# Performance work log

Hardware: AMD Instinct MI355X
Metric: run time of the kernel (lower is better)

## Reference

```python
import jax, jax.numpy as jnp
import numpy as np

M1, M2, M3 = 12, 12, 8
WIDTH = 32


def _spectral_conv(v, wr, wi):
    # v: [B, C, X, Y, T]; wr/wi: [4, Ci, Co, M1, M2, M3]
    B, C, X, Y, T = v.shape
    vft = jnp.fft.rfftn(v, axes=(-3, -2, -1))  # [B,C,X,Y,T//2+1] complex
    w = wr.astype(jnp.complex64) + 1j * wi.astype(jnp.complex64)
    mul = lambda blk, ww: jnp.einsum('bixyz,ioxyz->boxyz', blk, ww)
    out = jnp.zeros((B, wr.shape[2], X, Y, T // 2 + 1), dtype=vft.dtype)
    out = out.at[:, :, :M1, :M2, :M3].set(mul(vft[:, :, :M1, :M2, :M3], w[0]))
    out = out.at[:, :, -M1:, :M2, :M3].set(mul(vft[:, :, -M1:, :M2, :M3], w[1]))
    out = out.at[:, :, :M1, -M2:, :M3].set(mul(vft[:, :, :M1, -M2:, :M3], w[2]))
    out = out.at[:, :, -M1:, -M2:, :M3].set(mul(vft[:, :, -M1:, -M2:, :M3], w[3]))
    return jnp.fft.irfftn(out, s=(X, Y, T), axes=(-3, -2, -1))


def _conv1x1(v, w, b):
    # v: [B,C,X,Y,T]; w: [Co,Ci]; b: [Co]
    return jnp.einsum('bixyz,oi->boxyz', v, w) + b[None, :, None, None, None]


def setup_inputs() -> dict:
    key = jax.random.key(0)
    ks = jax.random.split(key, 24)
    B, X, Y, T = 8, 64, 64, 40
    W = WIDTH
    scale = 1.0 / (W * W)
    d = {}
    d['h'] = jax.random.normal(ks[0], (B, X, Y, T, 2), dtype=jnp.float32)
    d['x'] = jax.random.normal(ks[1], (B, X, Y, T, 3), dtype=jnp.float32)
    d['fc0_w'] = jax.random.normal(ks[2], (5, W), dtype=jnp.float32) * 0.3
    d['fc0_b'] = jnp.zeros((W,), dtype=jnp.float32)
    for i, name in enumerate(['sc0', 'sc1', 'sc3']):
        d[name + '_wr'] = scale * jax.random.uniform(ks[3 + 2 * i], (4, W, W, M1, M2, M3), dtype=jnp.float32)
        d[name + '_wi'] = scale * jax.random.uniform(ks[4 + 2 * i], (4, W, W, M1, M2, M3), dtype=jnp.float32)
    for i, name in enumerate(['w0', 'w1', 'w3']):
        d[name + '_w'] = jax.random.normal(ks[9 + 2 * i], (W, W), dtype=jnp.float32) * (1.0 / np.sqrt(W))
        d[name + '_b'] = jnp.zeros((W,), dtype=jnp.float32)
    d['fc1_w'] = jax.random.normal(ks[15], (W, 64), dtype=jnp.float32) * (1.0 / np.sqrt(W))
    d['fc1_b'] = jnp.zeros((64,), dtype=jnp.float32)
    d['fc2_w'] = jax.random.normal(ks[16], (64, 2), dtype=jnp.float32) * 0.125
    d['fc2_b'] = jnp.zeros((2,), dtype=jnp.float32)
    return d


def reference(h, x, fc0_w, fc0_b, sc0_wr, sc0_wi, sc1_wr, sc1_wi, sc3_wr, sc3_wi,
              w0_w, w0_b, w1_w, w1_b, w3_w, w3_b, fc1_w, fc1_b, fc2_w, fc2_b):
    v = jnp.concatenate((h, x), axis=-1)                 # [B,X,Y,T,5]
    v = v @ fc0_w + fc0_b                                # lift to width
    v = jnp.transpose(v, (0, 4, 1, 2, 3))                # [B,W,X,Y,T]
    v = jax.nn.gelu(_spectral_conv(v, sc0_wr, sc0_wi) + _conv1x1(v, w0_w, w0_b), approximate=False)
    v = jax.nn.gelu(_spectral_conv(v, sc1_wr, sc1_wi) + _conv1x1(v, w1_w, w1_b), approximate=False)
    v = _spectral_conv(v, sc3_wr, sc3_wi) + _conv1x1(v, w3_w, w3_b)
    v = jnp.transpose(v, (0, 2, 3, 4, 1))                # [B,X,Y,T,W]
    v = jax.nn.gelu(v @ fc1_w + fc1_b, approximate=False)
    return v @ fc2_w + fc2_b                             # [B,X,Y,T,2]
```

## Files before the change

### kernel.cpp

```cpp
#include <hip/hip_runtime.h>
#include <math.h>

#define BATCH 8
#define WID   32
#define NX    64
#define NY    64
#define NT    40
#define M1C   12
#define KT    8
#define KXC   24
#define KYC   24
#define NXY   (NX*NY)
#define NXYT  (NXY*NT)
#define NP    (BATCH*NXYT)

#define TWO_PI 6.283185307179586f

static __device__ __forceinline__ float gelu_f(float v){
  return 0.5f*v*(1.0f + erff(v*0.7071067811865476f));
}

static __device__ __forceinline__ void barrier_lds(){
  asm volatile("s_waitcnt lgkmcnt(0)\n\ts_barrier" ::: "memory");
}


__global__ __launch_bounds__(256) void k_fc0(const float* __restrict__ h, const float* __restrict__ x,
                                             const float* __restrict__ w, const float* __restrict__ b,
                                             float* __restrict__ V){
  __shared__ float sw[160], sb[32];
  int tid=threadIdx.x;
  if(tid<160) sw[tid]=w[tid];
  if(tid<32)  sb[tid]=b[tid];
  __syncthreads();
  int pl = tid>>3, q = tid&7;
  int p = blockIdx.x*32 + pl;
  float i0=h[(size_t)p*2], i1=h[(size_t)p*2+1];
  float i2=x[(size_t)p*3], i3=x[(size_t)p*3+1], i4=x[(size_t)p*3+2];
  int c0=q*4;
  float4 o;
  float* po=(float*)&o;
  #pragma unroll
  for(int u=0;u<4;u++){
    int c=c0+u;
    po[u] = sb[c] + i0*sw[c] + i1*sw[32+c] + i2*sw[64+c] + i3*sw[96+c] + i4*sw[128+c];
  }
  ((float4*)V)[(size_t)p*8 + q] = o;
}

__global__ __launch_bounds__(256) void k_fwd_ty(const float* __restrict__ V, float2* __restrict__ F2){
  __shared__ __align__(16) unsigned char smem[61696];
  float*  vt    = (float*)smem;
  float2* f2out = (float2*)smem;
  float2* twy   = (float2*)(smem + 49408);
  int tid = threadIdx.x;
  int b = blockIdx.x >> 6, x = blockIdx.x & 63;
  int c = tid & 31, k = tid >> 5;
  for(int i=tid;i<KYC*NY;i+=256){
    int ky=i/NY, y=i-ky*NY;
    int f = ky<M1C ? ky : ky+40;
    float ang = -TWO_PI*(float)((f*y)%NY)/(float)NY;
    twy[ky*NY+y] = make_float2(cosf(ang), sinf(ang));
  }
  float2 twr[NT];
  #pragma unroll
  for(int t=0;t<NT;t++){
    float ang = -TWO_PI*(float)((k*t)%NT)/(float)NT;
    twr[t] = make_float2(cosf(ang), sinf(ang));
  }
  float2 acc[KYC];
  #pragma unroll
  for(int ky=0;ky<KYC;ky++) acc[ky]=make_float2(0.f,0.f);
  const float4* src = (const float4*)(V + (size_t)(b*NX+x)*(NY*NT*WID));
  for(int g=0; g<8; g++){
    __syncthreads();
    #pragma unroll
    for(int r=0;r<10;r++) ((float4*)vt)[r*256+tid] = src[g*2560 + r*256 + tid];
    __syncthreads();
    for(int yl=0; yl<8; yl+=2){
      float sr0=0.f, si0=0.f, sr1=0.f, si1=0.f;
      const float* vp0 = vt + yl*1280 + c;
      const float* vp1 = vp0 + 1280;
      #pragma unroll
      for(int t=0;t<NT;t++){
        float2 w = twr[t];
        float v0 = vp0[t*32];
        float v1 = vp1[t*32];
        sr0 += v0*w.x; si0 += v0*w.y;
        sr1 += v1*w.x; si1 += v1*w.y;
      }
      int y = g*8 + yl;
      #pragma unroll
      for(int ky=0;ky<KYC;ky++){
        float4 wy = *(const float4*)&twy[ky*NY + y];
        acc[ky].x += sr0*wy.x - si0*wy.y + sr1*wy.z - si1*wy.w;
        acc[ky].y += sr0*wy.y + si0*wy.x + sr1*wy.w + si1*wy.z;
      }
    }
  }
  __syncthreads();
  #pragma unroll
  for(int ky=0;ky<KYC;ky++) f2out[c*193 + ky*KT + k] = acc[ky];
  __syncthreads();
  for(int i=tid;i<WID*KYC*KT;i+=256){
    int cc=i/192, e=i-cc*192;
    F2[((size_t)(b*WID+cc)*NX + x)*(KYC*KT) + e] = f2out[cc*193 + e];
  }
}

__global__ __launch_bounds__(256) void k_fwd_x(const float2* __restrict__ F2, float2* __restrict__ F3){
  __shared__ float2 tile[NX*KT];
  __shared__ float2 twi[KXC*65];
  int tid=threadIdx.x;
  int bc = blockIdx.x / KYC;
  int ky = blockIdx.x - bc*KYC;
  for(int i=tid;i<NX*KT;i+=256){
    int xx=i/KT, kt=i-xx*KT;
    tile[i] = F2[((size_t)bc*NX + xx)*(KYC*KT) + ky*KT + kt];
  }
  for(int i=tid;i<KXC*NX;i+=256){
    int kx=i/NX, xx=i-kx*NX;
    int f = kx<M1C ? kx : kx+40;
    float ang = -TWO_PI*(float)((f*xx)%NX)/(float)NX;
    twi[kx*65+xx] = make_float2(cosf(ang), sinf(ang));
  }
  __syncthreads();
  for(int item=tid; item<KXC*KT; item+=256){
    int kx=item/KT, kt=item-kx*KT;
    float sr=0.f, si=0.f;
    #pragma unroll 8
    for(int xx=0;xx<NX;xx++){
      float2 a = tile[xx*KT+kt];
      float2 w = twi[kx*65+xx];
      sr += a.x*w.x - a.y*w.y;
      si += a.x*w.y + a.y*w.x;
    }
    F3[(size_t)bc*(KXC*KYC*KT) + kx*(KYC*KT) + ky*KT + kt] = make_float2(sr,si);
  }
}

__global__ __launch_bounds__(256) void k_mix(const float2* __restrict__ F3, const float* __restrict__ wr,
                                             const float* __restrict__ wi, float2* __restrict__ F4){
  __shared__ float2 f3s[BATCH*WID*KT];
  int tid = threadIdx.x;
  int kx = blockIdx.x / KYC, ky = blockIdx.x - kx*KYC;
  int mode0 = blockIdx.x * KT;
  int xp = (kx>=M1C), yp = (ky>=M1C);
  int m1 = kx - M1C*xp, m2 = ky - M1C*yp;
  int blk = xp + 2*yp;
  for(int i=tid;i<1024;i+=256){
    int row=i>>2, q=i&3;
    ((float4*)f3s)[row*4+q] = ((const float4*)(F3 + (size_t)row*4608 + mode0))[q];
  }
  int o = tid>>3, kt = tid&7;
  size_t wbase = (size_t)blk*1179648 + (size_t)o*1152 + m1*96 + m2*8 + kt;
  float wre[WID], wim[WID];
  #pragma unroll
  for(int i=0;i<WID;i++){
    wre[i] = wr[wbase + (size_t)i*36864];
    wim[i] = wi[wbase + (size_t)i*36864];
  }
  __syncthreads();
  #pragma unroll
  for(int b=0;b<BATCH;b++){
    float ar=0.f, ai=0.f;
    #pragma unroll
    for(int i=0;i<WID;i++){
      float2 a = f3s[(b*WID+i)*KT + kt];
      ar += a.x*wre[i] - a.y*wim[i];
      ai += a.x*wim[i] + a.y*wre[i];
    }
    F4[(size_t)(b*WID+o)*4608 + mode0 + kt] = make_float2(ar,ai);
  }
}

__global__ __launch_bounds__(256) void k_inv_x(const float2* __restrict__ F4, float2* __restrict__ F2){
  __shared__ float2 tile[KXC*KT];
  __shared__ float2 twi[NX*25];
  int tid=threadIdx.x;
  int bc = blockIdx.x / KYC, ky = blockIdx.x - (blockIdx.x/KYC)*KYC;
  for(int i=tid;i<KXC*KT;i+=256){
    int kx=i/KT, kt=i-kx*KT;
    tile[i] = F4[(size_t)bc*4608 + kx*(KYC*KT) + ky*KT + kt];
  }
  for(int i=tid;i<NX*KXC;i+=256){
    int xx=i/KXC, kx=i-xx*KXC;
    int f = kx<M1C ? kx : kx+40;
    float ang = TWO_PI*(float)((f*xx)%NX)/(float)NX;
    twi[xx*25+kx] = make_float2(cosf(ang)*(1.0f/64.0f), sinf(ang)*(1.0f/64.0f));
  }
  __syncthreads();
  for(int item=tid; item<NX*KT; item+=256){
    int xx=item/KT, kt=item-xx*KT;
    float sr=0.f, si=0.f;
    #pragma unroll 8
    for(int kx=0;kx<KXC;kx++){
      float2 a = tile[kx*KT+kt];
      float2 w = twi[xx*25+kx];
      sr += a.x*w.x - a.y*w.y;
      si += a.x*w.y + a.y*w.x;
    }
    F2[((size_t)bc*NX + xx)*(KYC*KT) + ky*KT + kt] = make_float2(sr,si);
  }
}

template<bool GELU>
__global__ __launch_bounds__(256) void k_conv(const float2* __restrict__ F2, const float* __restrict__ wcv,
                                              const float* __restrict__ bcv, float* __restrict__ V){
  __shared__ __align__(16) unsigned char smem[34816];
  float*  vtA  = (float*)smem;
  float*  vtB  = (float*)(smem+10240);
  float2* ftc0 = (float2*)(smem+20480);
  float2* ftc1 = (float2*)(smem+24576);
  float2* twy  = (float2*)(smem+28672);
  float2* f2h  = (float2*)smem;

  int tid=threadIdx.x;
  int b  = blockIdx.x >> 7;
  int x  = (blockIdx.x >> 1) & 63;
  int y0 = (blockIdx.x & 1) * 32;
  int cid = tid & 31, ktid = tid >> 5;
  int oid = tid & 31, tg  = tid >> 5;

  float2 fr[KYC];
  #pragma unroll
  for(int half=0; half<2; half++){
    for(int i=tid;i<1536;i+=256){
      int cc=i/96, q=i-cc*96;
      ((float4*)f2h)[i] = *((const float4*)(F2 + ((size_t)(b*WID + half*16 + cc)*NX + x)*(KYC*KT)) + q);
    }
    __syncthreads();
    if((cid>>4) == half){
      const float2* fp = f2h + (cid&15)*192 + ktid;
      #pragma unroll
      for(int ky=0;ky<KYC;ky++) fr[ky] = fp[ky*8];
    }
    __syncthreads();
  }
  {
    float ts = (ktid==0 ? 1.0f : 2.0f) * (1.0f/(float)NT);
    #pragma unroll
    for(int ky=0;ky<KYC;ky++){ fr[ky].x *= ts; fr[ky].y *= ts; }
  }
  float wreg[WID];
  #pragma unroll
  for(int cc=0;cc<WID;cc++) wreg[cc] = wcv[oid*WID + cc];
  float breg = bcv[oid];
  float2 twtg[KT];
  #pragma unroll
  for(int k=0;k<KT;k++){
    float ang = 0.78539816339744831f*(float)((k*tg)&7);
    twtg[k] = make_float2(cosf(ang), sinf(ang));
  }
  for(int i=tid;i<32*KYC;i+=256){
    int yy=i/KYC, ky=i-yy*KYC;
    int f = ky<M1C ? ky : ky+40;
    float ang = TWO_PI*(float)((f*(y0+yy))%NY)/(float)NY;
    twy[i] = make_float2(cosf(ang)*(1.0f/64.0f), sinf(ang)*(1.0f/64.0f));
  }
  float* plane = V + (size_t)((b*NX+x)*NY + y0)*(NT*WID);
  const float4* gp = (const float4*)plane;
  bool has3 = tid < 128;
  {
    float4 p0 = gp[tid], p1 = gp[256+tid];
    float4 p2 = has3 ? gp[512+tid] : make_float4(0,0,0,0);
    ((float4*)vtA)[tid] = p0;
    ((float4*)vtA)[256+tid] = p1;
    if(has3) ((float4*)vtA)[512+tid] = p2;
  }
  float4 rA = gp[640+tid], rB = gp[640+256+tid];
  float4 rC = has3 ? gp[640+512+tid] : make_float4(0,0,0,0);
  __syncthreads();

  constexpr float CJ[KT][5] = {
    {1.f, 1.f,          1.f,          1.f,          1.f         },
    {1.f, 0.98768834f,  0.95105652f,  0.89100652f,  0.80901699f },
    {1.f, 0.95105652f,  0.80901699f,  0.58778525f,  0.30901699f },
    {1.f, 0.89100652f,  0.58778525f,  0.15643447f, -0.30901699f },
    {1.f, 0.80901699f,  0.30901699f, -0.30901699f, -0.80901699f },
    {1.f, 0.70710678f,  0.f,         -0.70710678f, -1.f         },
    {1.f, 0.58778525f, -0.30901699f, -0.95105652f, -0.80901699f },
    {1.f, 0.45399050f, -0.58778525f, -0.98768834f, -0.30901699f },
  };
  constexpr float SJ[KT][5] = {
    {0.f, 0.f,          0.f,          0.f,          0.f         },
    {0.f, 0.15643447f,  0.30901699f,  0.45399050f,  0.58778525f },
    {0.f, 0.30901699f,  0.58778525f,  0.80901699f,  0.95105652f },
    {0.f, 0.45399050f,  0.80901699f,  0.98768834f,  0.95105652f },
    {0.f, 0.58778525f,  0.95105652f,  0.95105652f,  0.58778525f },
    {0.f, 0.70710678f,  1.f,          0.70710678f,  0.f         },
    {0.f, 0.80901699f,  0.95105652f,  0.30901699f, -0.58778525f },
    {0.f, 0.89100652f,  0.80901699f, -0.15643447f, -0.95105652f },
  };

  #pragma unroll 1
  for(int it=0; it<16; ++it){
    float*  vcur = (it&1) ? vtB  : vtA;
    float*  vnxt = (it&1) ? vtA  : vtB;
    float2* fcur = (it&1) ? ftc1 : ftc0;
    int yl = it*2;
    {
      const float2* tw0 = twy + (size_t)yl*KYC;
      const float2* tw1 = tw0 + KYC;
      float sr0=0.f, si0=0.f, sr1=0.f, si1=0.f;
      #pragma unroll
      for(int ky=0;ky<KYC;ky+=2){
        float2 a  = fr[ky];
        float2 b2 = fr[ky+1];
        float4 w0 = *(const float4*)&tw0[ky];
        float4 w1 = *(const float4*)&tw1[ky];
        sr0 += a.x*w0.x - a.y*w0.y + b2.x*w0.z - b2.y*w0.w;
        si0 += a.x*w0.y + a.y*w0.x + b2.x*w0.w + b2.y*w0.z;
        sr1 += a.x*w1.x - a.y*w1.y + b2.x*w1.z - b2.y*w1.w;
        si1 += a.x*w1.y + a.y*w1.x + b2.x*w1.w + b2.y*w1.z;
      }
      fcur[      ktid*32 + cid] = make_float2(sr0,si0);
      fcur[256 + ktid*32 + cid] = make_float2(sr1,si1);
    }
    barrier_lds();
    if(it+1 < 16){
      ((float4*)vnxt)[tid] = rA;
      ((float4*)vnxt)[256+tid] = rB;
      if(has3) ((float4*)vnxt)[512+tid] = rC;
    }
    if(it+2 < 16){
      const float4* q = gp + (size_t)(it+2)*640;
      rA = q[tid]; rB = q[256+tid];
      if(has3) rC = q[512+tid];
    }
    #pragma unroll
    for(int yy=0; yy<2; yy++){
      const float2* fsrc = fcur + yy*256;
      const float*  vb   = vcur + yy*1280;
      float* outp = plane + (size_t)(yl+yy)*(NT*WID);
      float acc[5];
      #pragma unroll
      for(int j=0;j<5;j++) acc[j] = breg;
      #pragma unroll
      for(int k=0;k<KT;k++){
        float2 f = fsrc[k*32 + oid];
        float gx = f.x*twtg[k].x - f.y*twtg[k].y;
        float gy = f.x*twtg[k].y + f.y*twtg[k].x;
        #pragma unroll
        for(int j=0;j<5;j++) acc[j] += gx*CJ[k][j] - gy*SJ[k][j];
      }
      #pragma unroll
      for(int j=0;j<5;j++){
        int t = tg*5 + j;
        float a = acc[j];
        const float* vrow = vb + t*32;
        #pragma unroll
        for(int c4=0;c4<WID;c4+=4){
          float4 vv = *(const float4*)(vrow + c4);
          a += vv.x*wreg[c4] + vv.y*wreg[c4+1] + vv.z*wreg[c4+2] + vv.w*wreg[c4+3];
        }
        outp[t*32 + oid] = GELU ? gelu_f(a) : a;
      }
    }
  }
}

__global__ __launch_bounds__(256) void k_mlp(const float* __restrict__ V, const float* __restrict__ w1,
                                             const float* __restrict__ b1, const float* __restrict__ w2,
                                             const float* __restrict__ b2, float* __restrict__ out){
  __shared__ float sw1t[64*WID];
  __shared__ float sb1[64], sw2[128], sb2[2];
  int tid=threadIdx.x;
  for(int i=tid;i<64*WID;i+=256){ int j=i>>5, c=i&31; sw1t[i]=w1[c*64+j]; }
  if(tid<64) sb1[tid]=b1[tid];
  if(tid<128) sw2[tid]=w2[tid];
  if(tid<2) sb2[tid]=b2[tid];
  __syncthreads();
  size_t p0 = (size_t)blockIdx.x*1024 + (size_t)tid*4;
  float vv[128];
  const float4* vp = (const float4*)(V + p0*WID);
  #pragma unroll
  for(int q=0;q<32;q++) *((float4*)(vv+4*q)) = vp[q];
  float oa[8];
  #pragma unroll
  for(int pt=0;pt<4;pt++){ oa[2*pt]=sb2[0]; oa[2*pt+1]=sb2[1]; }
  #pragma unroll 4
  for(int j=0;j<64;j++){
    float a0=sb1[j], a1=a0, a2=a0, a3=a0;
    const float* wrow = sw1t + j*WID;
    #pragma unroll
    for(int c4=0;c4<WID;c4+=4){
      float4 w = *(const float4*)(wrow + c4);
      a0 += vv[     c4]*w.x + vv[     c4+1]*w.y + vv[     c4+2]*w.z + vv[     c4+3]*w.w;
      a1 += vv[32 + c4]*w.x + vv[32 + c4+1]*w.y + vv[32 + c4+2]*w.z + vv[32 + c4+3]*w.w;
      a2 += vv[64 + c4]*w.x + vv[64 + c4+1]*w.y + vv[64 + c4+2]*w.z + vv[64 + c4+3]*w.w;
      a3 += vv[96 + c4]*w.x + vv[96 + c4+1]*w.y + vv[96 + c4+2]*w.z + vv[96 + c4+3]*w.w;
    }
    a0=gelu_f(a0); a1=gelu_f(a1); a2=gelu_f(a2); a3=gelu_f(a3);
    float u0=sw2[2*j], u1=sw2[2*j+1];
    oa[0]+=a0*u0; oa[1]+=a0*u1; oa[2]+=a1*u0; oa[3]+=a1*u1;
    oa[4]+=a2*u0; oa[5]+=a2*u1; oa[6]+=a3*u0; oa[7]+=a3*u1;
  }
  float4* op = (float4*)(out + p0*2);
  op[0]=make_float4(oa[0],oa[1],oa[2],oa[3]);
  op[1]=make_float4(oa[4],oa[5],oa[6],oa[7]);
}

extern "C" void kernel_launch(void* const* d_in, const int* in_sizes, int n_in,
                              void* d_out, int out_size, void* d_ws, size_t ws_size,
                              hipStream_t stream){
  const float* h     = (const float*)d_in[0];
  const float* x     = (const float*)d_in[1];
  const float* fc0_w = (const float*)d_in[2];
  const float* fc0_b = (const float*)d_in[3];
  const float* scwr[3] = {(const float*)d_in[4], (const float*)d_in[6], (const float*)d_in[8]};
  const float* scwi[3] = {(const float*)d_in[5], (const float*)d_in[7], (const float*)d_in[9]};
  const float* cw[3]   = {(const float*)d_in[10], (const float*)d_in[12], (const float*)d_in[14]};
  const float* cb[3]   = {(const float*)d_in[11], (const float*)d_in[13], (const float*)d_in[15]};
  const float* fc1_w = (const float*)d_in[16];
  const float* fc1_b = (const float*)d_in[17];
  const float* fc2_w = (const float*)d_in[18];
  const float* fc2_b = (const float*)d_in[19];

  const size_t VSZ = (size_t)BATCH*WID*NXYT;
  float*  V  = (float*)d_ws;
  float2* F2 = (float2*)(V + VSZ);
  float2* F4 = F2 + (size_t)BATCH*WID*NX*KYC*KT;
  float2* F3 = (float2*)d_out;

  k_fc0<<<NP/32, 256, 0, stream>>>(h, x, fc0_w, fc0_b, V);
  for(int L=0; L<3; L++){
    k_fwd_ty<<<BATCH*NX, 256, 0, stream>>>(V, F2);
    k_fwd_x<<<(BATCH*WID)*KYC, 256, 0, stream>>>(F2, F3);
    k_mix<<<KXC*KYC, 256, 0, stream>>>(F3, scwr[L], scwi[L], F4);
    k_inv_x<<<(BATCH*WID)*KYC, 256, 0, stream>>>(F4, F2);
    if(L<2) k_conv<true ><<<BATCH*NX*2, 256, 0, stream>>>(F2, cw[L], cb[L], V);
    else    k_conv<false><<<BATCH*NX*2, 256, 0, stream>>>(F2, cw[L], cb[L], V);
  }
  k_mlp<<<NP/1024, 256, 0, stream>>>(V, fc1_w, fc1_b, fc2_w, fc2_b, (float*)d_out);
}
```

Before: 1.555 ms.

## Split forward T/Y DFT across ky halves and fold T symmetry

```diff
diff --git a/kernel.cpp b/kernel.cpp
--- a/kernel.cpp
+++ b/kernel.cpp
@@ -49,62 +49,65 @@
 }
 
 __global__ __launch_bounds__(256) void k_fwd_ty(const float* __restrict__ V, float2* __restrict__ F2){
-  __shared__ __align__(16) unsigned char smem[61696];
+  __shared__ __align__(16) unsigned char smem[26624];
   float*  vt    = (float*)smem;
+  float2* twy   = (float2*)(smem + 20480);
   float2* f2out = (float2*)smem;
-  float2* twy   = (float2*)(smem + 49408);
   int tid = threadIdx.x;
-  int b = blockIdx.x >> 6, x = blockIdx.x & 63;
+  int b = blockIdx.x >> 7, x = (blockIdx.x >> 1) & 63, kyh = blockIdx.x & 1;
   int c = tid & 31, k = tid >> 5;
-  for(int i=tid;i<KYC*NY;i+=256){
-    int ky=i/NY, y=i-ky*NY;
+  for(int i=tid;i<12*NY;i+=256){
+    int kyl=i>>6, y=i&63;
+    int ky = kyh*12 + kyl;
     int f = ky<M1C ? ky : ky+40;
     float ang = -TWO_PI*(float)((f*y)%NY)/(float)NY;
-    twy[ky*NY+y] = make_float2(cosf(ang), sinf(ang));
-  }
-  float2 twr[NT];
-  #pragma unroll
-  for(int t=0;t<NT;t++){
+    twy[i] = make_float2(cosf(ang), sinf(ang));
+  }
+  float2 twr[20];
+  #pragma unroll
+  for(int t=0;t<20;t++){
     float ang = -TWO_PI*(float)((k*t)%NT)/(float)NT;
     twr[t] = make_float2(cosf(ang), sinf(ang));
   }
-  float2 acc[KYC];
-  #pragma unroll
-  for(int ky=0;ky<KYC;ky++) acc[ky]=make_float2(0.f,0.f);
+  float sgn = (k&1) ? -1.0f : 1.0f;
+  float2 acc[12];
+  #pragma unroll
+  for(int q=0;q<12;q++) acc[q]=make_float2(0.f,0.f);
   const float4* src = (const float4*)(V + (size_t)(b*NX+x)*(NY*NT*WID));
-  for(int g=0; g<8; g++){
+  for(int g=0; g<16; g++){
     __syncthreads();
     #pragma unroll
-    for(int r=0;r<10;r++) ((float4*)vt)[r*256+tid] = src[g*2560 + r*256 + tid];
+    for(int r=0;r<5;r++) ((float4*)vt)[r*256+tid] = src[g*1280 + r*256 + tid];
     __syncthreads();
-    for(int yl=0; yl<8; yl+=2){
+    #pragma unroll
+    for(int yl=0; yl<4; yl+=2){
       float sr0=0.f, si0=0.f, sr1=0.f, si1=0.f;
       const float* vp0 = vt + yl*1280 + c;
       const float* vp1 = vp0 + 1280;
       #pragma unroll
-      for(int t=0;t<NT;t++){
+      for(int t=0;t<20;t++){
         float2 w = twr[t];
-        float v0 = vp0[t*32];
-        float v1 = vp1[t*32];
-        sr0 += v0*w.x; si0 += v0*w.y;
-        sr1 += v1*w.x; si1 += v1*w.y;
+        float u0 = fmaf(sgn, vp0[(t+20)*32], vp0[t*32]);
+        float u1 = fmaf(sgn, vp1[(t+20)*32], vp1[t*32]);
+        sr0 += u0*w.x; si0 += u0*w.y;
+        sr1 += u1*w.x; si1 += u1*w.y;
       }
-      int y = g*8 + yl;
-      #pragma unroll
-      for(int ky=0;ky<KYC;ky++){
-        float4 wy = *(const float4*)&twy[ky*NY + y];
-        acc[ky].x += sr0*wy.x - si0*wy.y + sr1*wy.z - si1*wy.w;
-        acc[ky].y += sr0*wy.y + si0*wy.x + sr1*wy.w + si1*wy.z;
+      int y = g*4 + yl;
+      #pragma unroll
+      for(int q=0;q<12;q++){
+        float4 wy = *(const float4*)&twy[q*NY + y];
+        acc[q].x += sr0*wy.x - si0*wy.y + sr1*wy.z - si1*wy.w;
+        acc[q].y += sr0*wy.y + si0*wy.x + sr1*wy.w + si1*wy.z;
       }
     }
   }
   __syncthreads();
   #pragma unroll
-  for(int ky=0;ky<KYC;ky++) f2out[c*193 + ky*KT + k] = acc[ky];
-  __syncthreads();
-  for(int i=tid;i<WID*KYC*KT;i+=256){
-    int cc=i/192, e=i-cc*192;
-    F2[((size_t)(b*WID+cc)*NX + x)*(KYC*KT) + e] = f2out[cc*193 + e];
+  for(int q=0;q<12;q++) f2out[c*97 + q*8 + k] = acc[q];
+  __syncthreads();
+  for(int i=tid;i<WID*96;i+=256){
+    int cc=i/96, e=i-cc*96;
+    F2[((size_t)(b*WID+cc)*NX + x)*(KYC*KT) + kyh*96 + e] = f2out[cc*97 + e];
   }
 }
 
@@ -425,7 +428,7 @@
 
   k_fc0<<<NP/32, 256, 0, stream>>>(h, x, fc0_w, fc0_b, V);
   for(int L=0; L<3; L++){
-    k_fwd_ty<<<BATCH*NX, 256, 0, stream>>>(V, F2);
+    k_fwd_ty<<<BATCH*NX*2, 256, 0, stream>>>(V, F2);
     k_fwd_x<<<(BATCH*WID)*KYC, 256, 0, stream>>>(F2, F3);
     k_mix<<<KXC*KYC, 256, 0, stream>>>(F3, scwr[L], scwi[L], F4);
     k_inv_x<<<(BATCH*WID)*KYC, 256, 0, stream>>>(F4, F2);
```

Result: slower. 1.603 ms (+3.1%).
